# Kernel optimization log

Measured on AMD Instinct MI355X. Metric: run time of the kernel, lower is better.

The kernel has to match this reference:

```python
import jax, jax.numpy as jnp
import numpy as np

D = 512
H = 8
W = 128  # window_size
HD = D // H
EPS = 1e-5


def _layernorm(x, g, b):
    mu = jnp.mean(x, axis=-1, keepdims=True)
    var = jnp.mean(jnp.square(x - mu), axis=-1, keepdims=True)
    return (x - mu) * jax.lax.rsqrt(var + EPS) * g + b


def setup_inputs() -> dict:
    key = jax.random.key(0)
    ks = jax.random.split(key, 6)
    B, S = 4, 8192
    src = jax.random.normal(ks[0], (B, S, D), jnp.float32)
    sc = 1.0 / np.sqrt(D)
    in_proj_w = jax.random.normal(ks[1], (3 * D, D), jnp.float32) * sc
    in_proj_b = jnp.zeros((3 * D,), jnp.float32)
    out_w = jax.random.normal(ks[2], (D, D), jnp.float32) * sc
    out_b = jnp.zeros((D,), jnp.float32)
    w1 = jax.random.normal(ks[3], (4 * D, D), jnp.float32) * sc
    b1 = jnp.zeros((4 * D,), jnp.float32)
    w2 = jax.random.normal(ks[4], (D, 4 * D), jnp.float32) * (1.0 / np.sqrt(4 * D))
    b2 = jnp.zeros((D,), jnp.float32)
    return {
        'src': src,
        'in_proj_w': in_proj_w, 'in_proj_b': in_proj_b,
        'out_w': out_w, 'out_b': out_b,
        'ln1_g': jnp.ones((D,), jnp.float32), 'ln1_b': jnp.zeros((D,), jnp.float32),
        'w1': w1, 'b1': b1, 'w2': w2, 'b2': b2,
        'ln2_g': jnp.ones((D,), jnp.float32), 'ln2_b': jnp.zeros((D,), jnp.float32),
    }


def reference(src, in_proj_w, in_proj_b, out_w, out_b, ln1_g, ln1_b,
              w1, b1, w2, b2, ln2_g, ln2_b):
    B, S, _ = src.shape
    nW = S // W
    x = src.reshape(B, nW, W, D)  # block-diagonal windows
    # packed qkv projection (torch MultiheadAttention in_proj)
    qkv = jnp.einsum('bnwd,ed->bnwe', x, in_proj_w) + in_proj_b
    q, k, v = jnp.split(qkv, 3, axis=-1)
    q = q.reshape(B, nW, W, H, HD)
    k = k.reshape(B, nW, W, H, HD)
    v = v.reshape(B, nW, W, H, HD)
    scores = jnp.einsum('bnqhd,bnkhd->bnhqk', q, k) / np.sqrt(HD)
    probs = jax.nn.softmax(scores, axis=-1)
    attn = jnp.einsum('bnhqk,bnkhd->bnqhd', probs, v).reshape(B, nW, W, D)
    attn = jnp.einsum('bnwd,ed->bnwe', attn, out_w) + out_b
    x = _layernorm(x + attn, ln1_g, ln1_b)
    ff = jnp.einsum('bnwf,df->bnwd', jax.nn.relu(jnp.einsum('bnwd,fd->bnwf', x, w1) + b1), w2) + b2
    x = _layernorm(x + ff, ln2_g, ln2_b)
    return x.reshape(B, S, D)
```

## Files before the change

### kernel.cpp

```cpp
#include <hip/hip_runtime.h>
#include <hip/hip_bf16.h>
#include <math.h>

typedef __bf16 bf16;
typedef bf16 bf16x8 __attribute__((ext_vector_type(8)));
typedef bf16 bf16x4 __attribute__((ext_vector_type(4)));
typedef float f32x4 __attribute__((ext_vector_type(4)));

#define MFMA16(a, b, c) __builtin_amdgcn_mfma_f32_16x16x32_bf16(a, b, c, 0, 0, 0)

__device__ __forceinline__ uint32_t swz(uint32_t base, uint32_t row, uint32_t rs, uint32_t cb) {
    return base + row * rs + (((cb >> 4) ^ (row & 7u)) << 4) + (cb & 15u);
}

__device__ __forceinline__ void gload16(const void* g, void* l) {
    __builtin_amdgcn_global_load_lds((const __attribute__((address_space(1))) void*)g,
                                     (__attribute__((address_space(3))) void*)l, 16, 0, 0);
}


__global__ void wcvt_kernel(const float* __restrict__ wqkv, const float* __restrict__ wout,
                            const float* __restrict__ w1f, const float* __restrict__ w2f,
                            bf16* __restrict__ o) {
    int i = blockIdx.x * blockDim.x + threadIdx.x;
    const float* s;
    int soff, doff;
    if (i < 98304) {
        int u = i;
        int tile = u >> 11, c = (u >> 9) & 3, nn = u & 511;
        int n = (tile >> 4) * 512 + nn;
        int k = (tile & 15) * 32 + c * 8;
        s = wqkv; soff = n * 512 + k; doff = u * 8;
    } else if (i < 131072) {
        int u = i - 98304;
        int tile = u >> 11, c = (u >> 9) & 3, nn = u & 511;
        int k = tile * 32 + c * 8;
        s = wout; soff = nn * 512 + k; doff = 786432 + u * 8;
    } else if (i < 262144) {
        int u = i - 131072;
        int tile = u >> 11, c = (u >> 9) & 3, nn = u & 511;
        int n = (tile >> 4) * 512 + nn;
        int k = (tile & 15) * 32 + c * 8;
        s = w1f; soff = n * 512 + k; doff = 1048576 + u * 8;
    } else {
        int u = i - 262144;
        int t = u >> 11, c = (u >> 9) & 3, nn = u & 511;
        int k = t * 32 + c * 8;
        s = w2f; soff = nn * 2048 + k; doff = 2097152 + u * 8;
    }
    float4 v0 = *(const float4*)(s + soff);
    float4 v1 = *(const float4*)(s + soff + 4);
    bf16x8 h = { (bf16)v0.x, (bf16)v0.y, (bf16)v0.z, (bf16)v0.w,
                 (bf16)v1.x, (bf16)v1.y, (bf16)v1.z, (bf16)v1.w };
    *(bf16x8*)(o + doff) = h;
}

__global__ void xcvt_kernel(float* __restrict__ src) {
    int row = blockIdx.x * 4 + (threadIdx.x >> 6);
    int l = threadIdx.x & 63;
    float* rp = src + (size_t)row * 512 + l * 8;
    float4 v0 = *(const float4*)rp;
    float4 v1 = *(const float4*)(rp + 4);
    asm volatile("s_waitcnt vmcnt(0)" ::: "memory");
    bf16x8 h = { (bf16)v0.x, (bf16)v0.y, (bf16)v0.z, (bf16)v0.w,
                 (bf16)v1.x, (bf16)v1.y, (bf16)v1.z, (bf16)v1.w };
    *(bf16x8*)((bf16*)(src + (size_t)row * 512) + l * 8) = h;
}

extern "C" __global__ __launch_bounds__(512, 2)
void qkv_kernel(const char* __restrict__ xb, const char* __restrict__ Wqkvp,
                const float* __restrict__ bqkv, char* __restrict__ qOb,
                char* __restrict__ kvb) {
    extern __shared__ char smem[];
    const int tid = threadIdx.x;
    const int w = tid >> 6, lane = tid & 63, l16 = lane & 15, quad = lane >> 4;
    const int wm = w >> 2, wn = w & 3;
    const int mb = blockIdx.x, cb = blockIdx.y;

    f32x4 acc[4][8];
#pragma unroll
    for (int i = 0; i < 4; ++i)
#pragma unroll
        for (int nt = 0; nt < 8; ++nt) acc[i][nt] = (f32x4){0.f, 0.f, 0.f, 0.f};

#define QKV_STAGE(buf, t)                                                              \
    {                                                                                  \
        int ca = w >> 1, rg = w & 1;           \
        gload16(xb + (size_t)(mb * 128 + rg * 64 + lane) * 2048 + (t) * 64 + ca * 16,  \
                smem + (uint32_t)(buf) * 8192u + ca * 2048 + rg * 1024);               \
        _Pragma("unroll")                                                              \
        for (int j = 0; j < 4; ++j) {      \
            int idx = w * 4 + j, c = idx >> 3, ng = idx & 7;                           \
            gload16(Wqkvp + (size_t)(cb * 16 + (t)) * 32768 + c * 8192 + ng * 1024 + lane * 16, \
                    smem + 16384u + (uint32_t)(buf) * 32768u + (uint32_t)c * 8192 + (uint32_t)ng * 1024); \
        }                                                                              \
    }

    QKV_STAGE(0, 0);
    __syncthreads();

#pragma unroll 1
    for (int t = 0; t < 16; ++t) {
        if (t < 15) QKV_STAGE((t + 1) & 1, t + 1);
        const uint32_t A0 = (uint32_t)(t & 1) * 8192u;
        const uint32_t B0 = 16384u + (uint32_t)(t & 1) * 32768u;
        bf16x8 a[4];
#pragma unroll
        for (int i = 0; i < 4; ++i)
            a[i] = *(const bf16x8*)(smem + A0 + quad * 2048 + (wm * 64 + i * 16 + l16) * 16);
#pragma unroll
        for (int nt = 0; nt < 8; ++nt) {
            bf16x8 b = *(const bf16x8*)(smem + B0 + quad * 8192 + (wn * 128 + nt * 16 + l16) * 16);
#pragma unroll
            for (int i = 0; i < 4; ++i) acc[i][nt] = MFMA16(a[i], b, acc[i][nt]);
        }
        __syncthreads();
    }
#undef QKV_STAGE

    const uint32_t sb = 16384u + (uint32_t)w * 4096u;
#pragma unroll
    for (int i = 0; i < 4; ++i) {
#pragma unroll
        for (int nt = 0; nt < 8; ++nt) {
            float bb = bqkv[cb * 512 + wn * 128 + nt * 16 + l16];
#pragma unroll
            for (int r = 0; r < 4; ++r)
                *(bf16*)(smem + swz(sb, quad * 4 + r, 256, (nt * 16 + l16) * 2)) =
                    (bf16)(acc[i][nt][r] + bb);
        }
        asm volatile("s_waitcnt lgkmcnt(0)" ::: "memory");
#pragma unroll
        for (int j = 0; j < 4; ++j) {
            int uu = j * 64 + lane;
            int row = uu >> 4, ch = uu & 15;
            bf16x8 v = *(bf16x8*)(smem + swz(sb, row, 256, ch * 16));
            size_t row_g = (size_t)(mb * 128 + wm * 64 + i * 16 + row);
            int nb2 = wn * 256 + ch * 16;
            if (cb == 0)      *(bf16x8*)(qOb + row_g * 1024 + nb2) = v;
            else if (cb == 1) *(bf16x8*)(kvb + row_g * 2048 + nb2) = v;
            else              *(bf16x8*)(kvb + row_g * 2048 + 1024 + nb2) = v;
        }
        asm volatile("s_waitcnt lgkmcnt(0)" ::: "memory");
    }
}

#define AVT 0u
#define ASCR 16384u
extern "C" __global__ __launch_bounds__(512, 4)
void attn_kernel(char* __restrict__ qOb, const char* __restrict__ kvb) {
    extern __shared__ char smem[];
    const int tid = threadIdx.x;
    const int wid = tid >> 6, lane = tid & 63, l16 = lane & 15, quad = lane >> 4;
    const int win = blockIdx.x >> 3, head = blockIdx.x & 7;
    const size_t wrow0 = (size_t)win * 128;
    f32x4 zero4 = { 0.f, 0.f, 0.f, 0.f };

    {
        int key = tid >> 2, d0 = (tid & 3) * 16;
        const char* vs = kvb + (wrow0 + key) * 2048 + 1024 + head * 128 + d0 * 2;
#pragma unroll
        for (int j = 0; j < 2; ++j) {
            bf16x8 v = *(const bf16x8*)(vs + j * 16);
#pragma unroll
            for (int e = 0; e < 8; ++e)
                *(bf16*)(smem + swz(AVT, d0 + j * 8 + e, 256, key * 2)) = v[e];
        }
    }
    __syncthreads();

    bf16x8 qf[2];
#pragma unroll
    for (int ks = 0; ks < 2; ++ks)
        qf[ks] = *(const bf16x8*)(qOb + (wrow0 + wid * 16 + l16) * 1024 + head * 128 + ks * 64 + quad * 16);

    f32x4 sa[8];
#pragma unroll
    for (int nt = 0; nt < 8; ++nt) sa[nt] = zero4;
#pragma unroll
    for (int nt = 0; nt < 8; ++nt)
#pragma unroll
        for (int ks = 0; ks < 2; ++ks) {
            bf16x8 kb = *(const bf16x8*)(kvb + (wrow0 + nt * 16 + l16) * 2048 + head * 128 + ks * 64 + quad * 16);
            sa[nt] = MFMA16(qf[ks], kb, sa[nt]);
        }
#pragma unroll
    for (int nt = 0; nt < 8; ++nt) sa[nt] *= 0.125f;
#pragma unroll
    for (int r = 0; r < 4; ++r) {
        float m = sa[0][r];
#pragma unroll
        for (int nt = 1; nt < 8; ++nt) m = fmaxf(m, sa[nt][r]);
#pragma unroll
        for (int sft = 1; sft < 16; sft <<= 1) m = fmaxf(m, __shfl_xor(m, sft, 64));
        float s = 0.f;
#pragma unroll
        for (int nt = 0; nt < 8; ++nt) {
            float e = __expf(sa[nt][r] - m);
            sa[nt][r] = e;
            s += e;
        }
#pragma unroll
        for (int sft = 1; sft < 16; sft <<= 1) s += __shfl_xor(s, sft, 64);
        float inv = 1.0f / s;
#pragma unroll
        for (int nt = 0; nt < 8; ++nt) sa[nt][r] *= inv;
    }

    const uint32_t sb = ASCR + (uint32_t)wid * 2048;
    bf16x8 pf[4];
#pragma unroll
    for (int hf = 0; hf < 2; ++hf) {
#pragma unroll
        for (int nt = 0; nt < 4; ++nt)
#pragma unroll
            for (int r = 0; r < 4; ++r)
                *(bf16*)(smem + swz(sb, quad * 4 + r, 128, (nt * 16 + l16) * 2)) = (bf16)sa[hf * 4 + nt][r];
        asm volatile("s_waitcnt lgkmcnt(0)" ::: "memory");
#pragma unroll
        for (int ks = 0; ks < 2; ++ks)
            pf[hf * 2 + ks] = *(bf16x8*)(smem + swz(sb, l16, 128, ks * 64 + quad * 16));
        asm volatile("s_waitcnt lgkmcnt(0)" ::: "memory");
    }

    f32x4 ov[4];
#pragma unroll
    for (int nt = 0; nt < 4; ++nt) {
        ov[nt] = zero4;
#pragma unroll
        for (int ks = 0; ks < 4; ++ks) {
            bf16x8 vb = *(bf16x8*)(smem + swz(AVT, nt * 16 + l16, 256, ks * 64 + quad * 16));
            ov[nt] = MFMA16(pf[ks], vb, ov[nt]);
        }
    }
#pragma unroll
    for (int hf = 0; hf < 2; ++hf) {
#pragma unroll
        for (int nt = 0; nt < 2; ++nt)
#pragma unroll
            for (int r = 0; r < 4; ++r)
                *(bf16*)(smem + swz(sb, quad * 4 + r, 128, (nt * 16 + l16) * 2)) = (bf16)ov[hf * 2 + nt][r];
        asm volatile("s_waitcnt lgkmcnt(0)" ::: "memory");
        {
            int row = lane >> 2, ch = lane & 3;
            bf16x8 v = *(bf16x8*)(smem + swz(sb, row, 128, ch * 16));
            *(bf16x8*)(qOb + (wrow0 + wid * 16 + row) * 1024 + head * 128 + hf * 64 + ch * 16) = v;
        }
        asm volatile("s_waitcnt lgkmcnt(0)" ::: "memory");
    }
}

extern "C" __global__ __launch_bounds__(512, 2)
void outproj_kernel(char* __restrict__ srcb, const char* __restrict__ qOb,
                    const char* __restrict__ Woutp, const float* __restrict__ bout,
                    const float* __restrict__ g1, const float* __restrict__ be1) {
    extern __shared__ char smem[];
    const int tid = threadIdx.x;
    const int w = tid >> 6, lane = tid & 63, l16 = lane & 15, quad = lane >> 4;
    const int wm = w >> 2, wn = w & 3;
    const int mb = blockIdx.x;

    f32x4 acc[4][8];
#pragma unroll
    for (int i = 0; i < 4; ++i)
#pragma unroll
        for (int nt = 0; nt < 8; ++nt) acc[i][nt] = (f32x4){0.f, 0.f, 0.f, 0.f};

#define OP_STAGE(buf, t)                                                               \
    {                                                                                  \
        int ca = w >> 1, rg = w & 1;           \
        gload16(qOb + (size_t)(mb * 128 + rg * 64 + lane) * 1024 + (t) * 64 + ca * 16, \
                smem + (uint32_t)(buf) * 8192u + ca * 2048 + rg * 1024);               \
        _Pragma("unroll")                                                              \
        for (int j = 0; j < 4; ++j) {      \
            int idx = w * 4 + j, c = idx >> 3, ng = idx & 7;                           \
            gload16(Woutp + (size_t)(t) * 32768 + c * 8192 + ng * 1024 + lane * 16,    \
                    smem + 16384u + (uint32_t)(buf) * 32768u + (uint32_t)c * 8192 + (uint32_t)ng * 1024); \
        }                                                                              \
    }

    OP_STAGE(0, 0);
    __syncthreads();

#pragma unroll 1
    for (int t = 0; t < 16; ++t) {
        if (t < 15) OP_STAGE((t + 1) & 1, t + 1);
        const uint32_t A0 = (uint32_t)(t & 1) * 8192u;
        const uint32_t B0 = 16384u + (uint32_t)(t & 1) * 32768u;
        bf16x8 a[4];
#pragma unroll
        for (int i = 0; i < 4; ++i)
            a[i] = *(const bf16x8*)(smem + A0 + quad * 2048 + (wm * 64 + i * 16 + l16) * 16);
#pragma unroll
        for (int nt = 0; nt < 8; ++nt) {
            bf16x8 b = *(const bf16x8*)(smem + B0 + quad * 8192 + (wn * 128 + nt * 16 + l16) * 16);
#pragma unroll
            for (int i = 0; i < 4; ++i) acc[i][nt] = MFMA16(a[i], b, acc[i][nt]);
        }
        __syncthreads();
    }
#undef OP_STAGE

#pragma unroll
    for (int nt = 0; nt < 8; ++nt) {
        int col = wn * 128 + nt * 16 + l16;
        float bb = bout[col];
#pragma unroll
        for (int i = 0; i < 4; ++i)
#pragma unroll
            for (int r = 0; r < 4; ++r) {
                int row = mb * 128 + wm * 64 + i * 16 + quad * 4 + r;
                float xv = (float)*(const bf16*)(srcb + (size_t)row * 2048 + col * 2);
                acc[i][nt][r] += bb + xv;
            }
    }
    float ps[4][4], ps2[4][4];
#pragma unroll
    for (int i = 0; i < 4; ++i)
#pragma unroll
        for (int r = 0; r < 4; ++r) {
            float s = 0.f, s2 = 0.f;
#pragma unroll
            for (int nt = 0; nt < 8; ++nt) {
                float v = acc[i][nt][r];
                s += v;
                s2 += v * v;
            }
#pragma unroll
            for (int sft = 1; sft < 16; sft <<= 1) {
                s += __shfl_xor(s, sft, 64);
                s2 += __shfl_xor(s2, sft, 64);
            }
            ps[i][r] = s;
            ps2[i][r] = s2;
        }
    if (l16 == 0) {
#pragma unroll
        for (int i = 0; i < 4; ++i)
#pragma unroll
            for (int r = 0; r < 4; ++r) {
                int row_l = wm * 64 + i * 16 + quad * 4 + r;
                *(float*)(smem + row_l * 32 + wn * 8) = ps[i][r];
                *(float*)(smem + row_l * 32 + wn * 8 + 4) = ps2[i][r];
            }
    }
    __syncthreads();
    const uint32_t sb = 16384u + (uint32_t)w * 4096u;
#pragma unroll
    for (int i = 0; i < 4; ++i) {
#pragma unroll
        for (int r = 0; r < 4; ++r) {
            int row_l = wm * 64 + i * 16 + quad * 4 + r;
            float S = 0.f, S2 = 0.f;
#pragma unroll
            for (int w4 = 0; w4 < 4; ++w4) {
                S += *(const float*)(smem + row_l * 32 + w4 * 8);
                S2 += *(const float*)(smem + row_l * 32 + w4 * 8 + 4);
            }
            float mu = S * (1.0f / 512.0f);
            float var = S2 * (1.0f / 512.0f) - mu * mu;
            float rstd = rsqrtf(var + 1e-5f);
#pragma unroll
            for (int nt = 0; nt < 8; ++nt) {
                int col = wn * 128 + nt * 16 + l16;
                float v = (acc[i][nt][r] - mu) * rstd * g1[col] + be1[col];
                *(bf16*)(smem + swz(sb, quad * 4 + r, 256, (nt * 16 + l16) * 2)) = (bf16)v;
            }
        }
        asm volatile("s_waitcnt lgkmcnt(0)" ::: "memory");
#pragma unroll
        for (int j = 0; j < 4; ++j) {
            int uu = j * 64 + lane;
            int row = uu >> 4, ch = uu & 15;
            bf16x8 v = *(bf16x8*)(smem + swz(sb, row, 256, ch * 16));
            *(bf16x8*)(srcb + (size_t)(mb * 128 + wm * 64 + i * 16 + row) * 2048 + 1024 +
                       wn * 256 + ch * 16) = v;
        }
        asm volatile("s_waitcnt lgkmcnt(0)" ::: "memory");
    }
}

extern "C" __global__ __launch_bounds__(512, 2)
void ff1_kernel(char* __restrict__ srcb, const char* __restrict__ W1p,
                const float* __restrict__ b1, char* __restrict__ doutb,
                char* __restrict__ wsOb) {
    extern __shared__ char smem[];
    const int tid = threadIdx.x;
    const int w = tid >> 6, lane = tid & 63, l16 = lane & 15, quad = lane >> 4;
    const int wm = w >> 2, wn = w & 3;
    const int mb = blockIdx.x, cb = blockIdx.y;

    f32x4 acc[4][8];
#pragma unroll
    for (int i = 0; i < 4; ++i)
#pragma unroll
        for (int nt = 0; nt < 8; ++nt) acc[i][nt] = (f32x4){0.f, 0.f, 0.f, 0.f};

#define FF1_STAGE(buf, t)                                                              \
    {                                                                                  \
        int ca = w >> 1, rg = w & 1;             \
        gload16(srcb + (size_t)(mb * 128 + rg * 64 + lane) * 2048 + 1024 + (t) * 64 + ca * 16, \
                smem + (uint32_t)(buf) * 8192u + ca * 2048 + rg * 1024);               \
        _Pragma("unroll")                                                              \
        for (int j = 0; j < 4; ++j) {      \
            int idx = w * 4 + j, c = idx >> 3, ng = idx & 7;                           \
            gload16(W1p + (size_t)(cb * 16 + (t)) * 32768 + c * 8192 + ng * 1024 + lane * 16, \
                    smem + 16384u + (uint32_t)(buf) * 32768u + (uint32_t)c * 8192 + (uint32_t)ng * 1024); \
        }                                                                              \
    }

    FF1_STAGE(0, 0);
    __syncthreads();

#pragma unroll 1
    for (int t = 0; t < 16; ++t) {
        if (t < 15) FF1_STAGE((t + 1) & 1, t + 1);
        const uint32_t A0 = (uint32_t)(t & 1) * 8192u;
        const uint32_t B0 = 16384u + (uint32_t)(t & 1) * 32768u;
        bf16x8 a[4];
#pragma unroll
        for (int i = 0; i < 4; ++i)
            a[i] = *(const bf16x8*)(smem + A0 + quad * 2048 + (wm * 64 + i * 16 + l16) * 16);
#pragma unroll
        for (int nt = 0; nt < 8; ++nt) {
            bf16x8 b = *(const bf16x8*)(smem + B0 + quad * 8192 + (wn * 128 + nt * 16 + l16) * 16);
#pragma unroll
            for (int i = 0; i < 4; ++i) acc[i][nt] = MFMA16(a[i], b, acc[i][nt]);
        }
        __syncthreads();
    }
#undef FF1_STAGE

    const uint32_t sb = 16384u + (uint32_t)w * 4096u;
#pragma unroll
    for (int i = 0; i < 4; ++i) {
#pragma unroll
        for (int nt = 0; nt < 8; ++nt) {
            float bb = b1[cb * 512 + wn * 128 + nt * 16 + l16];
#pragma unroll
            for (int r = 0; r < 4; ++r)
                *(bf16*)(smem + swz(sb, quad * 4 + r, 256, (nt * 16 + l16) * 2)) =
                    (bf16)fmaxf(acc[i][nt][r] + bb, 0.0f);
        }
        asm volatile("s_waitcnt lgkmcnt(0)" ::: "memory");
#pragma unroll
        for (int j = 0; j < 4; ++j) {
            int uu = j * 64 + lane;
            int row = uu >> 4, ch = uu & 15;
            bf16x8 v = *(bf16x8*)(smem + swz(sb, row, 256, ch * 16));
            size_t row_g = (size_t)(mb * 128 + wm * 64 + i * 16 + row);
            int nb2 = wn * 256 + ch * 16;
            if (cb < 2)       *(bf16x8*)(doutb + row_g * 2048 + cb * 1024 + nb2) = v;
            else if (cb == 2) *(bf16x8*)(srcb + row_g * 2048 + nb2) = v;
            else              *(bf16x8*)(wsOb + row_g * 1024 + nb2) = v;
        }
        asm volatile("s_waitcnt lgkmcnt(0)" ::: "memory");
    }
}

extern "C" __global__ __launch_bounds__(512, 2)
void ff2_kernel(char* __restrict__ doutb, const char* __restrict__ srcb,
                const char* __restrict__ wsOb, const char* __restrict__ W2p,
                const float* __restrict__ b2, const float* __restrict__ g2,
                const float* __restrict__ be2) {
    extern __shared__ char smem[];
    const int tid = threadIdx.x;
    const int w = tid >> 6, lane = tid & 63, l16 = lane & 15, quad = lane >> 4;
    const int wm = w >> 2, wn = w & 3;
    const int mb = blockIdx.x;

    f32x4 acc[4][8];
#pragma unroll
    for (int i = 0; i < 4; ++i)
#pragma unroll
        for (int nt = 0; nt < 8; ++nt) acc[i][nt] = (f32x4){0.f, 0.f, 0.f, 0.f};

#define FF2_STAGE(buf, t)                                                              \
    {                                                                                  \
        const char* hb; int rstride, koffb;                                            \
        if ((t) < 32)      { hb = doutb; rstride = 2048; koffb = (t) * 64; }           \
        else if ((t) < 48) { hb = srcb;  rstride = 2048; koffb = ((t) - 32) * 64; }    \
        else               { hb = wsOb;  rstride = 1024; koffb = ((t) - 48) * 64; }    \
        int ca = w >> 1, rg = w & 1;           \
        gload16(hb + (size_t)(mb * 128 + rg * 64 + lane) * rstride + koffb + ca * 16,  \
                smem + (uint32_t)(buf) * 8192u + ca * 2048 + rg * 1024);               \
        _Pragma("unroll")                                                              \
        for (int j = 0; j < 4; ++j) {      \
            int idx = w * 4 + j, c = idx >> 3, ng = idx & 7;                           \
            gload16(W2p + (size_t)(t) * 32768 + c * 8192 + ng * 1024 + lane * 16,      \
                    smem + 16384u + (uint32_t)(buf) * 32768u + (uint32_t)c * 8192 + (uint32_t)ng * 1024); \
        }                                                                              \
    }

    FF2_STAGE(0, 0);
    __syncthreads();

#pragma unroll 1
    for (int t = 0; t < 64; ++t) {
        if (t < 63) FF2_STAGE((t + 1) & 1, t + 1);
        const uint32_t A0 = (uint32_t)(t & 1) * 8192u;
        const uint32_t B0 = 16384u + (uint32_t)(t & 1) * 32768u;
        bf16x8 a[4];
#pragma unroll
        for (int i = 0; i < 4; ++i)
            a[i] = *(const bf16x8*)(smem + A0 + quad * 2048 + (wm * 64 + i * 16 + l16) * 16);
#pragma unroll
        for (int nt = 0; nt < 8; ++nt) {
            bf16x8 b = *(const bf16x8*)(smem + B0 + quad * 8192 + (wn * 128 + nt * 16 + l16) * 16);
#pragma unroll
            for (int i = 0; i < 4; ++i) acc[i][nt] = MFMA16(a[i], b, acc[i][nt]);
        }
        __syncthreads();
    }
#undef FF2_STAGE

#pragma unroll
    for (int nt = 0; nt < 8; ++nt) {
        int col = wn * 128 + nt * 16 + l16;
        float bb = b2[col];
#pragma unroll
        for (int i = 0; i < 4; ++i)
#pragma unroll
            for (int r = 0; r < 4; ++r) {
                int row = mb * 128 + wm * 64 + i * 16 + quad * 4 + r;
                float x1v = (float)*(const bf16*)(srcb + (size_t)row * 2048 + 1024 + col * 2);
                acc[i][nt][r] += bb + x1v;
            }
    }
    float ps[4][4], ps2[4][4];
#pragma unroll
    for (int i = 0; i < 4; ++i)
#pragma unroll
        for (int r = 0; r < 4; ++r) {
            float s = 0.f, s2 = 0.f;
#pragma unroll
            for (int nt = 0; nt < 8; ++nt) {
                float v = acc[i][nt][r];
                s += v;
                s2 += v * v;
            }
#pragma unroll
            for (int sft = 1; sft < 16; sft <<= 1) {
                s += __shfl_xor(s, sft, 64);
                s2 += __shfl_xor(s2, sft, 64);
            }
            ps[i][r] = s;
            ps2[i][r] = s2;
        }
    if (l16 == 0) {
#pragma unroll
        for (int i = 0; i < 4; ++i)
#pragma unroll
            for (int r = 0; r < 4; ++r) {
                int row_l = wm * 64 + i * 16 + quad * 4 + r;
                *(float*)(smem + row_l * 32 + wn * 8) = ps[i][r];
                *(float*)(smem + row_l * 32 + wn * 8 + 4) = ps2[i][r];
            }
    }
    __syncthreads();
#pragma unroll
    for (int i = 0; i < 4; ++i)
#pragma unroll
        for (int r = 0; r < 4; ++r) {
            int row_l = wm * 64 + i * 16 + quad * 4 + r;
            float S = 0.f, S2 = 0.f;
#pragma unroll
            for (int w4 = 0; w4 < 4; ++w4) {
                S += *(const float*)(smem + row_l * 32 + w4 * 8);
                S2 += *(const float*)(smem + row_l * 32 + w4 * 8 + 4);
            }
            float mu = S * (1.0f / 512.0f);
            float var = S2 * (1.0f / 512.0f) - mu * mu;
            float rstd = rsqrtf(var + 1e-5f);
            size_t row = (size_t)(mb * 128 + row_l);
#pragma unroll
            for (int nt = 0; nt < 8; ++nt) {
                int col = wn * 128 + nt * 16 + l16;
                *(float*)(doutb + row * 2048 + col * 4) =
                    (acc[i][nt][r] - mu) * rstd * g2[col] + be2[col];
            }
        }
}

extern "C" void kernel_launch(void* const* d_in, const int* in_sizes, int n_in,
                              void* d_out, int out_size, void* d_ws, size_t ws_size,
                              hipStream_t stream) {
    (void)in_sizes; (void)n_in; (void)out_size; (void)ws_size;
    float* src = (float*)d_in[0];
    const float* ipw = (const float*)d_in[1];
    const float* ipb = (const float*)d_in[2];
    const float* ow  = (const float*)d_in[3];
    const float* ob  = (const float*)d_in[4];
    const float* g1  = (const float*)d_in[5];
    const float* be1 = (const float*)d_in[6];
    const float* w1  = (const float*)d_in[7];
    const float* b1  = (const float*)d_in[8];
    const float* w2  = (const float*)d_in[9];
    const float* b2  = (const float*)d_in[10];
    const float* g2  = (const float*)d_in[11];
    const float* be2 = (const float*)d_in[12];
    bf16* ws = (bf16*)d_ws;
    char* srcb = (char*)src;
    char* doutb = (char*)d_out;
    char* qOb = (char*)d_ws + 6291456;

    wcvt_kernel<<<1536, 256, 0, stream>>>(ipw, ow, w1, w2, ws);
    xcvt_kernel<<<8192, 256, 0, stream>>>(src);

    hipFuncSetAttribute((const void*)qkv_kernel, hipFuncAttributeMaxDynamicSharedMemorySize, 81920);
    hipFuncSetAttribute((const void*)attn_kernel, hipFuncAttributeMaxDynamicSharedMemorySize, 32768);
    hipFuncSetAttribute((const void*)outproj_kernel, hipFuncAttributeMaxDynamicSharedMemorySize, 81920);
    hipFuncSetAttribute((const void*)ff1_kernel, hipFuncAttributeMaxDynamicSharedMemorySize, 81920);
    hipFuncSetAttribute((const void*)ff2_kernel, hipFuncAttributeMaxDynamicSharedMemorySize, 81920);

    qkv_kernel<<<dim3(256, 3), 512, 81920, stream>>>(srcb, (const char*)ws, ipb, qOb, doutb);
    attn_kernel<<<2048, 512, 32768, stream>>>(qOb, doutb);
    outproj_kernel<<<256, 512, 81920, stream>>>(srcb, qOb, (const char*)(ws + 786432), ob, g1, be1);
    ff1_kernel<<<dim3(256, 4), 512, 81920, stream>>>(srcb, (const char*)(ws + 1048576), b1, doutb, qOb);
    ff2_kernel<<<256, 512, 81920, stream>>>(doutb, srcb, qOb, (const char*)(ws + 2097152), b2, g2, be2);
}
```

Baseline: 524.4 us.

## Triple-buffer LDS staging with explicit vmcnt waits in GEMM kernels

Converts the double-buffered global-to-LDS pipeline in the qkv, outproj, ff1 and ff2 GEMM kernels to a three-stage ring. Loads now run two K-steps ahead, and `__syncthreads` is replaced by a partial `s_waitcnt vmcnt` plus a raw barrier, so one stage's loads can stay in flight across the barrier. The goal is to hide more global-load latency behind MFMA work. The cost is dynamic LDS growing from 80KB to 120KB per block. That likely allows only one 512-thread block per CU instead of two, which hurts the kernels with more blocks than CUs (qkv, ff1).

Measured after the change: 497.3 us. -5.2%, faster.

```diff
diff --git a/kernel.cpp b/kernel.cpp
--- a/kernel.cpp
+++ b/kernel.cpp
@@ -17,6 +17,7 @@
     __builtin_amdgcn_global_load_lds((const __attribute__((address_space(1))) void*)g,
                                      (__attribute__((address_space(3))) void*)l, 16, 0, 0);
 }
+
 
 
 __global__ void wcvt_kernel(const float* __restrict__ wqkv, const float* __restrict__ wout,
@@ -83,27 +84,31 @@
 #pragma unroll
         for (int nt = 0; nt < 8; ++nt) acc[i][nt] = (f32x4){0.f, 0.f, 0.f, 0.f};
 
-#define QKV_STAGE(buf, t)                                                              \
+#define QKV_STAGE(ib, t)                                                               \
     {                                                                                  \
         int ca = w >> 1, rg = w & 1;           \
         gload16(xb + (size_t)(mb * 128 + rg * 64 + lane) * 2048 + (t) * 64 + ca * 16,  \
-                smem + (uint32_t)(buf) * 8192u + ca * 2048 + rg * 1024);               \
+                smem + (uint32_t)(ib) * 8192u + ca * 2048 + rg * 1024);                \
         _Pragma("unroll")                                                              \
         for (int j = 0; j < 4; ++j) {      \
             int idx = w * 4 + j, c = idx >> 3, ng = idx & 7;                           \
             gload16(Wqkvp + (size_t)(cb * 16 + (t)) * 32768 + c * 8192 + ng * 1024 + lane * 16, \
-                    smem + 16384u + (uint32_t)(buf) * 32768u + (uint32_t)c * 8192 + (uint32_t)ng * 1024); \
+                    smem + 24576u + (uint32_t)(ib) * 32768u + (uint32_t)c * 8192 + (uint32_t)ng * 1024); \
         }                                                                              \
     }
 
     QKV_STAGE(0, 0);
-    __syncthreads();
-
+    QKV_STAGE(1, 1);
+    asm volatile("s_waitcnt vmcnt(5)" ::: "memory");
+    __builtin_amdgcn_s_barrier();
+
+    int ib = 0;
 #pragma unroll 1
     for (int t = 0; t < 16; ++t) {
-        if (t < 15) QKV_STAGE((t + 1) & 1, t + 1);
-        const uint32_t A0 = (uint32_t)(t & 1) * 8192u;
-        const uint32_t B0 = 16384u + (uint32_t)(t & 1) * 32768u;
+        int in2 = ib + 2; if (in2 >= 3) in2 -= 3;
+        if (t + 2 < 16) QKV_STAGE(in2, t + 2);
+        const uint32_t A0 = (uint32_t)ib * 8192u;
+        const uint32_t B0 = 24576u + (uint32_t)ib * 32768u;
         bf16x8 a[4];
 #pragma unroll
         for (int i = 0; i < 4; ++i)
@@ -114,11 +119,14 @@
 #pragma unroll
             for (int i = 0; i < 4; ++i) acc[i][nt] = MFMA16(a[i], b, acc[i][nt]);
         }
-        __syncthreads();
+        if (t + 2 < 16) asm volatile("s_waitcnt vmcnt(5)" ::: "memory");
+        else            asm volatile("s_waitcnt vmcnt(0)" ::: "memory");
+        __builtin_amdgcn_s_barrier();
+        ib = (ib == 2) ? 0 : ib + 1;
     }
 #undef QKV_STAGE
 
-    const uint32_t sb = 16384u + (uint32_t)w * 4096u;
+    const uint32_t sb = 24576u + (uint32_t)w * 4096u;
 #pragma unroll
     for (int i = 0; i < 4; ++i) {
 #pragma unroll
@@ -266,27 +274,31 @@
 #pragma unroll
         for (int nt = 0; nt < 8; ++nt) acc[i][nt] = (f32x4){0.f, 0.f, 0.f, 0.f};
 
-#define OP_STAGE(buf, t)                                                               \
+#define OP_STAGE(ib, t)                                                                \
     {                                                                                  \
         int ca = w >> 1, rg = w & 1;           \
         gload16(qOb + (size_t)(mb * 128 + rg * 64 + lane) * 1024 + (t) * 64 + ca * 16, \
-                smem + (uint32_t)(buf) * 8192u + ca * 2048 + rg * 1024);               \
+                smem + (uint32_t)(ib) * 8192u + ca * 2048 + rg * 1024);                \
         _Pragma("unroll")                                                              \
         for (int j = 0; j < 4; ++j) {      \
             int idx = w * 4 + j, c = idx >> 3, ng = idx & 7;                           \
             gload16(Woutp + (size_t)(t) * 32768 + c * 8192 + ng * 1024 + lane * 16,    \
-                    smem + 16384u + (uint32_t)(buf) * 32768u + (uint32_t)c * 8192 + (uint32_t)ng * 1024); \
+                    smem + 24576u + (uint32_t)(ib) * 32768u + (uint32_t)c * 8192 + (uint32_t)ng * 1024); \
         }                                                                              \
     }
 
     OP_STAGE(0, 0);
-    __syncthreads();
-
+    OP_STAGE(1, 1);
+    asm volatile("s_waitcnt vmcnt(5)" ::: "memory");
+    __builtin_amdgcn_s_barrier();
+
+    int ib = 0;
 #pragma unroll 1
     for (int t = 0; t < 16; ++t) {
-        if (t < 15) OP_STAGE((t + 1) & 1, t + 1);
-        const uint32_t A0 = (uint32_t)(t & 1) * 8192u;
-        const uint32_t B0 = 16384u + (uint32_t)(t & 1) * 32768u;
+        int in2 = ib + 2; if (in2 >= 3) in2 -= 3;
+        if (t + 2 < 16) OP_STAGE(in2, t + 2);
+        const uint32_t A0 = (uint32_t)ib * 8192u;
+        const uint32_t B0 = 24576u + (uint32_t)ib * 32768u;
         bf16x8 a[4];
 #pragma unroll
         for (int i = 0; i < 4; ++i)
@@ -297,7 +309,10 @@
 #pragma unroll
             for (int i = 0; i < 4; ++i) acc[i][nt] = MFMA16(a[i], b, acc[i][nt]);
         }
-        __syncthreads();
+        if (t + 2 < 16) asm volatile("s_waitcnt vmcnt(5)" ::: "memory");
+        else            asm volatile("s_waitcnt vmcnt(0)" ::: "memory");
+        __builtin_amdgcn_s_barrier();
+        ib = (ib == 2) ? 0 : ib + 1;
     }
 #undef OP_STAGE
 
@@ -345,7 +360,7 @@
             }
     }
     __syncthreads();
-    const uint32_t sb = 16384u + (uint32_t)w * 4096u;
+    const uint32_t sb = 24576u + (uint32_t)w * 4096u;
 #pragma unroll
     for (int i = 0; i < 4; ++i) {
 #pragma unroll
@@ -396,27 +411,31 @@
 #pragma unroll
         for (int nt = 0; nt < 8; ++nt) acc[i][nt] = (f32x4){0.f, 0.f, 0.f, 0.f};
 
-#define FF1_STAGE(buf, t)                                                              \
+#define FF1_STAGE(ib, t)                                                               \
     {                                                                                  \
         int ca = w >> 1, rg = w & 1;             \
         gload16(srcb + (size_t)(mb * 128 + rg * 64 + lane) * 2048 + 1024 + (t) * 64 + ca * 16, \
-                smem + (uint32_t)(buf) * 8192u + ca * 2048 + rg * 1024);               \
+                smem + (uint32_t)(ib) * 8192u + ca * 2048 + rg * 1024);                \
         _Pragma("unroll")                                                              \
         for (int j = 0; j < 4; ++j) {      \
             int idx = w * 4 + j, c = idx >> 3, ng = idx & 7;                           \
             gload16(W1p + (size_t)(cb * 16 + (t)) * 32768 + c * 8192 + ng * 1024 + lane * 16, \
-                    smem + 16384u + (uint32_t)(buf) * 32768u + (uint32_t)c * 8192 + (uint32_t)ng * 1024); \
+                    smem + 24576u + (uint32_t)(ib) * 32768u + (uint32_t)c * 8192 + (uint32_t)ng * 1024); \
         }                                                                              \
     }
 
     FF1_STAGE(0, 0);
-    __syncthreads();
-
+    FF1_STAGE(1, 1);
+    asm volatile("s_waitcnt vmcnt(5)" ::: "memory");
+    __builtin_amdgcn_s_barrier();
+
+    int ib = 0;
 #pragma unroll 1
     for (int t = 0; t < 16; ++t) {
-        if (t < 15) FF1_STAGE((t + 1) & 1, t + 1);
-        const uint32_t A0 = (uint32_t)(t & 1) * 8192u;
-        const uint32_t B0 = 16384u + (uint32_t)(t & 1) * 32768u;
+        int in2 = ib + 2; if (in2 >= 3) in2 -= 3;
+        if (t + 2 < 16) FF1_STAGE(in2, t + 2);
+        const uint32_t A0 = (uint32_t)ib * 8192u;
+        const uint32_t B0 = 24576u + (uint32_t)ib * 32768u;
         bf16x8 a[4];
 #pragma unroll
         for (int i = 0; i < 4; ++i)
@@ -427,11 +446,14 @@
 #pragma unroll
             for (int i = 0; i < 4; ++i) acc[i][nt] = MFMA16(a[i], b, acc[i][nt]);
         }
-        __syncthreads();
+        if (t + 2 < 16) asm volatile("s_waitcnt vmcnt(5)" ::: "memory");
+        else            asm volatile("s_waitcnt vmcnt(0)" ::: "memory");
+        __builtin_amdgcn_s_barrier();
+        ib = (ib == 2) ? 0 : ib + 1;
     }
 #undef FF1_STAGE
 
-    const uint32_t sb = 16384u + (uint32_t)w * 4096u;
+    const uint32_t sb = 24576u + (uint32_t)w * 4096u;
 #pragma unroll
     for (int i = 0; i < 4; ++i) {
 #pragma unroll
@@ -475,7 +497,7 @@
 #pragma unroll
         for (int nt = 0; nt < 8; ++nt) acc[i][nt] = (f32x4){0.f, 0.f, 0.f, 0.f};
 
-#define FF2_STAGE(buf, t)                                                              \
+#define FF2_STAGE(ib, t)                                                               \
     {                                                                                  \
         const char* hb; int rstride, koffb;                                            \
         if ((t) < 32)      { hb = doutb; rstride = 2048; koffb = (t) * 64; }           \
@@ -483,23 +505,27 @@
         else               { hb = wsOb;  rstride = 1024; koffb = ((t) - 48) * 64; }    \
         int ca = w >> 1, rg = w & 1;           \
         gload16(hb + (size_t)(mb * 128 + rg * 64 + lane) * rstride + koffb + ca * 16,  \
-                smem + (uint32_t)(buf) * 8192u + ca * 2048 + rg * 1024);               \
+                smem + (uint32_t)(ib) * 8192u + ca * 2048 + rg * 1024);                \
         _Pragma("unroll")                                                              \
         for (int j = 0; j < 4; ++j) {      \
             int idx = w * 4 + j, c = idx >> 3, ng = idx & 7;                           \
             gload16(W2p + (size_t)(t) * 32768 + c * 8192 + ng * 1024 + lane * 16,      \
-                    smem + 16384u + (uint32_t)(buf) * 32768u + (uint32_t)c * 8192 + (uint32_t)ng * 1024); \
+                    smem + 24576u + (uint32_t)(ib) * 32768u + (uint32_t)c * 8192 + (uint32_t)ng * 1024); \
         }                                                                              \
     }
 
     FF2_STAGE(0, 0);
-    __syncthreads();
-
+    FF2_STAGE(1, 1);
+    asm volatile("s_waitcnt vmcnt(5)" ::: "memory");
+    __builtin_amdgcn_s_barrier();
+
+    int ib = 0;
 #pragma unroll 1
     for (int t = 0; t < 64; ++t) {
-        if (t < 63) FF2_STAGE((t + 1) & 1, t + 1);
-        const uint32_t A0 = (uint32_t)(t & 1) * 8192u;
-        const uint32_t B0 = 16384u + (uint32_t)(t & 1) * 32768u;
+        int in2 = ib + 2; if (in2 >= 3) in2 -= 3;
+        if (t + 2 < 64) FF2_STAGE(in2, t + 2);
+        const uint32_t A0 = (uint32_t)ib * 8192u;
+        const uint32_t B0 = 24576u + (uint32_t)ib * 32768u;
         bf16x8 a[4];
 #pragma unroll
         for (int i = 0; i < 4; ++i)
@@ -510,7 +536,10 @@
 #pragma unroll
             for (int i = 0; i < 4; ++i) acc[i][nt] = MFMA16(a[i], b, acc[i][nt]);
         }
-        __syncthreads();
+        if (t + 2 < 64) asm volatile("s_waitcnt vmcnt(5)" ::: "memory");
+        else            asm volatile("s_waitcnt vmcnt(0)" ::: "memory");
+        __builtin_amdgcn_s_barrier();
+        ib = (ib == 2) ? 0 : ib + 1;
     }
 #undef FF2_STAGE
 
@@ -607,15 +636,15 @@
     wcvt_kernel<<<1536, 256, 0, stream>>>(ipw, ow, w1, w2, ws);
     xcvt_kernel<<<8192, 256, 0, stream>>>(src);
 
-    hipFuncSetAttribute((const void*)qkv_kernel, hipFuncAttributeMaxDynamicSharedMemorySize, 81920);
+    hipFuncSetAttribute((const void*)qkv_kernel, hipFuncAttributeMaxDynamicSharedMemorySize, 122880);
     hipFuncSetAttribute((const void*)attn_kernel, hipFuncAttributeMaxDynamicSharedMemorySize, 32768);
-    hipFuncSetAttribute((const void*)outproj_kernel, hipFuncAttributeMaxDynamicSharedMemorySize, 81920);
-    hipFuncSetAttribute((const void*)ff1_kernel, hipFuncAttributeMaxDynamicSharedMemorySize, 81920);
-    hipFuncSetAttribute((const void*)ff2_kernel, hipFuncAttributeMaxDynamicSharedMemorySize, 81920);
-
-    qkv_kernel<<<dim3(256, 3), 512, 81920, stream>>>(srcb, (const char*)ws, ipb, qOb, doutb);
+    hipFuncSetAttribute((const void*)outproj_kernel, hipFuncAttributeMaxDynamicSharedMemorySize, 122880);
+    hipFuncSetAttribute((const void*)ff1_kernel, hipFuncAttributeMaxDynamicSharedMemorySize, 122880);
+    hipFuncSetAttribute((const void*)ff2_kernel, hipFuncAttributeMaxDynamicSharedMemorySize, 122880);
+
+    qkv_kernel<<<dim3(256, 3), 512, 122880, stream>>>(srcb, (const char*)ws, ipb, qOb, doutb);
     attn_kernel<<<2048, 512, 32768, stream>>>(qOb, doutb);
-    outproj_kernel<<<256, 512, 81920, stream>>>(srcb, qOb, (const char*)(ws + 786432), ob, g1, be1);
-    ff1_kernel<<<dim3(256, 4), 512, 81920, stream>>>(srcb, (const char*)(ws + 1048576), b1, doutb, qOb);
-    ff2_kernel<<<256, 512, 81920, stream>>>(doutb, srcb, qOb, (const char*)(ws + 2097152), b2, g2, be2);
-}
+    outproj_kernel<<<256, 512, 122880, stream>>>(srcb, qOb, (const char*)(ws + 786432), ob, g1, be1);
+    ff1_kernel<<<dim3(256, 4), 512, 122880, stream>>>(srcb, (const char*)(ws + 1048576), b1, doutb, qOb);
+    ff2_kernel<<<256, 512, 122880, stream>>>(doutb, srcb, qOb, (const char*)(ws + 2097152), b2, g2, be2);
+}
```
